# Kernel tuning notes

Hardware: AMD Instinct MI355X
Metric: run time of the kernel (lower is better)

Reference implementation:

```python
import jax, jax.numpy as jnp
import numpy as np

NUM_EMBEDDINGS = 1024
EMBEDDING_DIM = 256
COMMITMENT_COST = 0.25
DECAY = 0.99
EPSILON = 1e-05


def setup_inputs() -> dict:
    key = jax.random.key(0)
    k1, k2, k3 = jax.random.split(key, 3)
    z_e = jax.random.normal(k1, (32, 32, 32, EMBEDDING_DIM), dtype=jnp.float32)
    embedding = jax.random.normal(k2, (NUM_EMBEDDINGS, EMBEDDING_DIM), dtype=jnp.float32)
    ema_cluster_size = jnp.zeros((NUM_EMBEDDINGS,), dtype=jnp.float32)
    ema_w = jax.random.normal(k3, (NUM_EMBEDDINGS, EMBEDDING_DIM), dtype=jnp.float32)
    return {"z_e": z_e, "embedding": embedding,
            "ema_cluster_size": ema_cluster_size, "ema_w": ema_w}


def reference(z_e, embedding, ema_cluster_size, ema_w):
    K, D = embedding.shape
    flat = z_e.reshape(-1, D)  # [N, D]
    distances = (jnp.sum(flat * flat, axis=1, keepdims=True)
                 - 2.0 * (flat @ embedding.T)
                 + jnp.sum(embedding * embedding, axis=1))
    encoding_indices = jnp.argmin(distances, axis=1)  # [N]
    # one_hot @ embedding == gather of nearest codes
    z_q = embedding[encoding_indices].reshape(z_e.shape)

    # EMA codebook update (training branch, torch no_grad)
    counts = jax.ops.segment_sum(jnp.ones_like(encoding_indices, dtype=flat.dtype),
                                 encoding_indices, num_segments=K)  # encodings.sum(0)
    dw = jax.ops.segment_sum(flat, encoding_indices, num_segments=K)  # encodings.T @ flat
    new_cluster_size = DECAY * ema_cluster_size + (1.0 - DECAY) * counts
    new_ema_w = DECAY * ema_w + (1.0 - DECAY) * dw
    n = jnp.sum(new_cluster_size)
    cluster_size = (new_cluster_size + EPSILON) / (n + K * EPSILON) * n
    new_embedding = new_ema_w / cluster_size[:, None]

    codebook_loss = jnp.mean((z_q - jax.lax.stop_gradient(z_e)) ** 2)
    commitment_loss = COMMITMENT_COST * jnp.mean((z_e - jax.lax.stop_gradient(z_q)) ** 2)
    vq_loss = codebook_loss + commitment_loss
    z_q_st = z_e + jax.lax.stop_gradient(z_q - z_e)  # straight-through
    return (z_q_st, vq_loss, encoding_indices,
            new_embedding, new_cluster_size, new_ema_w)
```

## Files before the change

kernel.cpp:

```cpp
#include <hip/hip_runtime.h>

#define DECAY_F 0.99f
#define OMD_F   0.01f
#define EPS_F   1e-5f

typedef __attribute__((ext_vector_type(8)))  __bf16 bf16x8;
typedef __attribute__((ext_vector_type(16))) float  f32x16;

#define WSB_CNTI     0
#define WSB_LOSS     4096
#define WSB_DWACC    8192
#define WSB_CSUM     1056768
#define WSB_ENORM    1056832
#define WSB_IDX      1060928
#define WSB_EHI      1192000
#define WSB_ELO      1716288
#define WSB_SORT     2240576
#define WSB_CURS     2371648

#define OUT_ZQ    0
#define OUT_LOSS  8388608
#define OUT_IDX   8388609
#define OUT_EMB   8421377
#define OUT_CS    8683521
#define OUT_EMAW  8684545

__device__ __forceinline__ unsigned short f2bf(float x) {
    unsigned u = __builtin_bit_cast(unsigned, x);
    u += 0x7fffu + ((u >> 16) & 1u);
    return (unsigned short)(u >> 16);
}
__device__ __forceinline__ float bf2f(unsigned short h) {
    return __builtin_bit_cast(float, (unsigned)h << 16);
}
__device__ __forceinline__ void split8(const float4 a, const float4 b,
                                       uint4& hi, uint4& lo) {
    float f[8] = {a.x, a.y, a.z, a.w, b.x, b.y, b.z, b.w};
    unsigned short h[8], l[8];
    #pragma unroll
    for (int i = 0; i < 8; ++i) {
        h[i] = f2bf(f[i]);
        l[i] = f2bf(f[i] - bf2f(h[i]));
    }
    hi.x = (unsigned)h[0] | ((unsigned)h[1] << 16);
    hi.y = (unsigned)h[2] | ((unsigned)h[3] << 16);
    hi.z = (unsigned)h[4] | ((unsigned)h[5] << 16);
    hi.w = (unsigned)h[6] | ((unsigned)h[7] << 16);
    lo.x = (unsigned)l[0] | ((unsigned)l[1] << 16);
    lo.y = (unsigned)l[2] | ((unsigned)l[3] << 16);
    lo.z = (unsigned)l[4] | ((unsigned)l[5] << 16);
    lo.w = (unsigned)l[6] | ((unsigned)l[7] << 16);
}

__global__ __launch_bounds__(256)
void esplit_enorm_kernel(const float* __restrict__ emb,
                         unsigned short* __restrict__ e_hi,
                         unsigned short* __restrict__ e_lo,
                         float* __restrict__ enorm,
                         float* __restrict__ dwacc,
                         int* __restrict__ cnt,
                         float* __restrict__ lossbuf) {
    const int tid = threadIdx.x, lane = tid & 63, wv = tid >> 6;
    const int gthread = blockIdx.x * 256 + tid;

    *(float4*)(dwacc + (size_t)gthread * 4) = make_float4(0.f, 0.f, 0.f, 0.f);
    if (gthread < 1024) cnt[gthread] = 0;
    if (gthread < 256)  lossbuf[gthread] = 0.f;

    if (gthread < 32768) {
        const int F     = gthread;
        const int chunk = F >> 6;
        const int lh6   = (F >> 5) & 1;
        const int l31f  = F & 31;
        const int g     = chunk >> 4;
        const int kc    = (chunk >> 1) & 7;
        const int kk    = chunk & 1;
        const int k     = g * 32 + l31f;
        const int d0    = kc * 32 + (kk * 2 + lh6) * 8;
        const float4 v0 = *(const float4*)(emb + (size_t)k * 256 + d0);
        const float4 v1 = *(const float4*)(emb + (size_t)k * 256 + d0 + 4);
        uint4 h, l;
        split8(v0, v1, h, l);
        *(uint4*)((char*)e_hi + (size_t)F * 16) = h;
        *(uint4*)((char*)e_lo + (size_t)F * 16) = l;
    }

    const int k = blockIdx.x * 4 + wv;
    const float4 v = *(const float4*)(emb + (size_t)k * 256 + lane * 4);
    float s = v.x * v.x + v.y * v.y + v.z * v.z + v.w * v.w;
    #pragma unroll
    for (int off = 32; off > 0; off >>= 1) s += __shfl_down(s, off);
    if (lane == 0) enorm[k] = s;
}

__global__ __launch_bounds__(256, 2)
void argmin_kernel(const float* __restrict__ z,
                   const unsigned short* __restrict__ e_hi,
                   const unsigned short* __restrict__ e_lo,
                   const float* __restrict__ enorm,
                   const float* __restrict__ emb,
                   int* __restrict__ idx, float* __restrict__ idxf,
                   float* __restrict__ out_zq, int* __restrict__ cnt) {
    __shared__ unsigned short Ah[32 * 512], Al[32 * 512];

    const int tid  = threadIdx.x;
    const int lane = tid & 63;
    const int wv   = tid >> 6;
    const int l31  = lane & 31, lh = lane >> 5;
    const int row0 = blockIdx.x * 64;

    #pragma unroll
    for (int c8 = 0; c8 < 8; ++c8) {
        const int C  = wv * 8 + c8;
        const int i  = C >> 4, kc = (C >> 1) & 7, kk = C & 1;
        const int row = row0 + i * 32 + l31;
        const int d0  = kc * 32 + (kk * 2 + lh) * 8;
        const float4 v0 = *(const float4*)(z + (size_t)row * 256 + d0);
        const float4 v1 = *(const float4*)(z + (size_t)row * 256 + d0 + 4);
        uint4 h, l;
        split8(v0, v1, h, l);
        *(uint4*)((char*)Ah + (size_t)C * 1024 + lane * 16) = h;
        *(uint4*)((char*)Al + (size_t)C * 1024 + lane * 16) = l;
    }
    __syncthreads();

    f32x16 acc[2][2];
    #pragma unroll
    for (int i = 0; i < 2; ++i)
        #pragma unroll
        for (int j = 0; j < 2; ++j) acc[i][j] = (f32x16)0.0f;

    float bestd[2][16];
    int   besti[2][16];
    #pragma unroll
    for (int i = 0; i < 2; ++i)
        #pragma unroll
        for (int r = 0; r < 16; ++r) { bestd[i][r] = 3.4e38f; besti[i][r] = 0; }

    uint4 b0h[4], b0l[4], b1h[4], b1l[4];
    auto loadB = [&](int s, uint4* bh, uint4* bl) {
        const int csp = s >> 3, kc = s & 7;
        #pragma unroll
        for (int j = 0; j < 2; ++j)
            #pragma unroll
            for (int kk = 0; kk < 2; ++kk) {
                const int chunk = (csp * 8 + wv * 2 + j) * 16 + kc * 2 + kk;
                bh[j * 2 + kk] = *(const uint4*)((const char*)e_hi + (size_t)chunk * 1024 + lane * 16);
                bl[j * 2 + kk] = *(const uint4*)((const char*)e_lo + (size_t)chunk * 1024 + lane * 16);
            }
    };
    auto compute = [&](int s, const uint4* bh4, const uint4* bl4) {
        const int kc = s & 7;
        #pragma unroll
        for (int kk = 0; kk < 2; ++kk) {
            bf16x8 bh[2], bl[2];
            #pragma unroll
            for (int j = 0; j < 2; ++j) {
                bh[j] = __builtin_bit_cast(bf16x8, bh4[j * 2 + kk]);
                bl[j] = __builtin_bit_cast(bf16x8, bl4[j * 2 + kk]);
            }
            #pragma unroll
            for (int i = 0; i < 2; ++i) {
                const int C = i * 16 + kc * 2 + kk;
                const bf16x8 ah = __builtin_bit_cast(bf16x8,
                    *(const uint4*)((const char*)Ah + (size_t)C * 1024 + lane * 16));
                const bf16x8 al = __builtin_bit_cast(bf16x8,
                    *(const uint4*)((const char*)Al + (size_t)C * 1024 + lane * 16));
                #pragma unroll
                for (int j = 0; j < 2; ++j) {
                    acc[i][j] = __builtin_amdgcn_mfma_f32_32x32x16_bf16(ah, bh[j], acc[i][j], 0, 0, 0);
                    acc[i][j] = __builtin_amdgcn_mfma_f32_32x32x16_bf16(al, bh[j], acc[i][j], 0, 0, 0);
                    acc[i][j] = __builtin_amdgcn_mfma_f32_32x32x16_bf16(ah, bl[j], acc[i][j], 0, 0, 0);
                }
            }
        }
        if ((s & 7) == 7) {
            const int csp = s >> 3;
            #pragma unroll
            for (int j = 0; j < 2; ++j) {
                const int col = csp * 256 + wv * 64 + j * 32 + l31;
                const float en = enorm[col];
                #pragma unroll
                for (int i = 0; i < 2; ++i)
                    #pragma unroll
                    for (int r = 0; r < 16; ++r) {
                        const float d = fmaf(-2.0f, acc[i][j][r], en);
                        if (d < bestd[i][r] || (d == bestd[i][r] && col < besti[i][r])) {
                            bestd[i][r] = d; besti[i][r] = col;
                        }
                    }
            }
            #pragma unroll
            for (int i = 0; i < 2; ++i)
                #pragma unroll
                for (int j = 0; j < 2; ++j) acc[i][j] = (f32x16)0.0f;
        }
    };

    loadB(0, b0h, b0l);
    for (int s = 0; s < 32; s += 2) {
        loadB(s + 1, b1h, b1l);
        compute(s, b0h, b0l);
        if (s + 2 < 32) loadB(s + 2, b0h, b0l);
        compute(s + 1, b1h, b1l);
    }

    #pragma unroll
    for (int m = 1; m < 32; m <<= 1) {
        #pragma unroll
        for (int i = 0; i < 2; ++i)
            #pragma unroll
            for (int r = 0; r < 16; ++r) {
                const float od = __shfl_xor(bestd[i][r], m);
                const int   oi = __shfl_xor(besti[i][r], m);
                if (od < bestd[i][r] || (od == bestd[i][r] && oi < besti[i][r])) {
                    bestd[i][r] = od; besti[i][r] = oi;
                }
            }
    }

    __syncthreads();
    float* mg_d = (float*)Ah;
    int*   mg_i = (int*)Ah + 256;
    if (l31 == 0) {
        #pragma unroll
        for (int i = 0; i < 2; ++i)
            #pragma unroll
            for (int r = 0; r < 16; ++r) {
                const int rloc = i * 32 + (r & 3) + 8 * (r >> 2) + 4 * lh;
                mg_d[wv * 64 + rloc] = bestd[i][r];
                mg_i[wv * 64 + rloc] = besti[i][r];
            }
    }
    __syncthreads();
    if (tid < 64) {
        float d0 = mg_d[tid];
        int   i0 = mg_i[tid];
        #pragma unroll
        for (int w = 1; w < 4; ++w) {
            const float dw = mg_d[w * 64 + tid];
            const int   iw = mg_i[w * 64 + tid];
            if (dw < d0 || (dw == d0 && iw < i0)) { d0 = dw; i0 = iw; }
        }
        const int n = row0 + tid;
        idx[n] = i0; idxf[n] = (float)i0;
        atomicAdd(&cnt[i0], 1);
        mg_i[tid] = i0;
    }
    __syncthreads();

    #pragma unroll 4
    for (int r = 0; r < 16; ++r) {
        const int row = wv * 16 + r;
        const int code = mg_i[row];
        const float4 e4 = *(const float4*)(emb + (size_t)code * 256 + lane * 4);
        *(float4*)(out_zq + (size_t)(row0 + row) * 256 + lane * 4) = e4;
    }
}

__global__ __launch_bounds__(1024)
void scan_kernel(const float* __restrict__ ema_cs, const int* __restrict__ cnt,
                 float* __restrict__ out_cs, float* __restrict__ csum,
                 int* __restrict__ cursor) {
    __shared__ int   wtmp[16];
    __shared__ float wred[16];
    const int t = threadIdx.x, lane = t & 63, wv = t >> 6;
    const int c = cnt[t];
    const float f = DECAY_F * ema_cs[t] + OMD_F * (float)c;
    out_cs[t] = f;
    float fs = f;
    #pragma unroll
    for (int o = 32; o > 0; o >>= 1) fs += __shfl_down(fs, o);
    if (lane == 0) wred[wv] = fs;
    int v = c;
    #pragma unroll
    for (int o = 1; o < 64; o <<= 1) { const int u = __shfl_up(v, o); if (lane >= o) v += u; }
    if (lane == 63) wtmp[wv] = v;
    __syncthreads();
    if (t == 0) { float s2 = 0.f; for (int w = 0; w < 16; ++w) s2 += wred[w]; csum[0] = s2; }
    int wbase = 0;
    #pragma unroll
    for (int w = 0; w < 16; ++w) if (w < wv) wbase += wtmp[w];
    cursor[t] = wbase + v - c;
}

__global__ __launch_bounds__(256)
void scatter_kernel(const int* __restrict__ idx, int* __restrict__ cursor,
                    int* __restrict__ sorted) {
    const int n = blockIdx.x * 256 + threadIdx.x;
    const int k = idx[n];
    const int p = atomicAdd(&cursor[k], 1);
    sorted[p] = n;
}

__global__ __launch_bounds__(256)
void dw_kernel(const float* __restrict__ z, const float* __restrict__ emb,
               const float* __restrict__ enorm,
               const int* __restrict__ sorted, const int* __restrict__ idx,
               float* __restrict__ dwacc, float* __restrict__ lossbuf) {
    const int lane = threadIdx.x & 63;
    const int w    = blockIdx.x * 4 + (threadIdx.x >> 6);
    const int r0   = w * 16;
    const int srow = sorted[r0 + (lane & 15)];
    const int skey = idx[srow];

    float4 s = make_float4(0.f, 0.f, 0.f, 0.f);
    float sumsq = 0.f;
    int cntr = 0;
    int krun = __shfl(skey, 0);

    auto flush = [&](int k) {
        const float4 e = *(const float4*)(emb + (size_t)k * 256 + lane * 4);
        float val = sumsq - 2.0f * (e.x * s.x + e.y * s.y + e.z * s.z + e.w * s.w);
        #pragma unroll
        for (int off = 32; off > 0; off >>= 1) val += __shfl_down(val, off);
        if (lane == 0) atomicAdd(&lossbuf[k & 255], val + (float)cntr * enorm[k]);
        float* p = dwacc + (size_t)k * 256 + lane * 4;
        atomicAdd(p + 0, s.x); atomicAdd(p + 1, s.y);
        atomicAdd(p + 2, s.z); atomicAdd(p + 3, s.w);
    };

    #pragma unroll 8
    for (int j = 0; j < 16; ++j) {
        const int row = __shfl(srow, j);
        const int k   = __shfl(skey, j);
        if (k != krun) {
            flush(krun);
            s = make_float4(0.f, 0.f, 0.f, 0.f);
            sumsq = 0.f; cntr = 0; krun = k;
        }
        const float4 v = *(const float4*)(z + (size_t)row * 256 + lane * 4);
        s.x += v.x; s.y += v.y; s.z += v.z; s.w += v.w;
        sumsq += v.x * v.x + v.y * v.y + v.z * v.z + v.w * v.w;
        ++cntr;
    }
    flush(krun);
}

__global__ __launch_bounds__(256)
void update_w_kernel(const float* __restrict__ ema_w, const float* __restrict__ dwacc,
                     const float* __restrict__ out_cs, const float* __restrict__ csum,
                     const float* __restrict__ lossbuf,
                     float* __restrict__ out_emb, float* __restrict__ out_emaw,
                     float* __restrict__ out_loss) {
    __shared__ float red[256];
    const int t = threadIdx.x;
    if (blockIdx.x == 0) {
        red[t] = lossbuf[t]; __syncthreads();
        #pragma unroll
        for (int off = 128; off > 0; off >>= 1) {
            if (t < off) red[t] += red[t + off];
            __syncthreads();
        }
        if (t == 0) out_loss[0] = 1.25f * red[0] / 8388608.0f;
    }

    const int g = blockIdx.x * 256 + t;
    const int k = g >> 6;
    const float n_total = csum[0];
    const float cs = (out_cs[k] + EPS_F) / (n_total + 1024.0f * EPS_F) * n_total;

    const float4 w4 = *(const float4*)(ema_w + (size_t)g * 4);
    const float4 d4 = *(const float4*)(dwacc + (size_t)g * 4);
    float4 nw, ne;
    nw.x = DECAY_F * w4.x + OMD_F * d4.x;
    nw.y = DECAY_F * w4.y + OMD_F * d4.y;
    nw.z = DECAY_F * w4.z + OMD_F * d4.z;
    nw.w = DECAY_F * w4.w + OMD_F * d4.w;
    ne.x = nw.x / cs; ne.y = nw.y / cs; ne.z = nw.z / cs; ne.w = nw.w / cs;
    *(float4*)(out_emaw + (size_t)g * 4) = nw;
    *(float4*)(out_emb  + (size_t)g * 4) = ne;
}

extern "C" void kernel_launch(void* const* d_in, const int* in_sizes, int n_in,
                              void* d_out, int out_size, void* d_ws, size_t ws_size,
                              hipStream_t stream) {
    const float* z      = (const float*)d_in[0];
    const float* emb    = (const float*)d_in[1];
    const float* ema_cs = (const float*)d_in[2];
    const float* ema_w  = (const float*)d_in[3];

    float* out = (float*)d_out;
    char*  wsb = (char*)d_ws;

    int*            cnt     = (int*)(wsb + WSB_CNTI);
    float*          lossbuf = (float*)(wsb + WSB_LOSS);
    float*          dwacc   = (float*)(wsb + WSB_DWACC);
    float*          csum    = (float*)(wsb + WSB_CSUM);
    float*          enorm   = (float*)(wsb + WSB_ENORM);
    int*            idx     = (int*)(wsb + WSB_IDX);
    unsigned short* e_hi    = (unsigned short*)(wsb + WSB_EHI);
    unsigned short* e_lo    = (unsigned short*)(wsb + WSB_ELO);
    int*            sorted  = (int*)(wsb + WSB_SORT);
    int*            cursor  = (int*)(wsb + WSB_CURS);

    float* out_zq   = out + OUT_ZQ;
    float* out_loss = out + OUT_LOSS;
    float* out_idxf = out + OUT_IDX;
    float* out_emb  = out + OUT_EMB;
    float* out_cs   = out + OUT_CS;
    float* out_emaw = out + OUT_EMAW;

    esplit_enorm_kernel<<<256, 256, 0, stream>>>(emb, e_hi, e_lo, enorm,
                                                 dwacc, cnt, lossbuf);
    argmin_kernel<<<512, 256, 0, stream>>>(z, e_hi, e_lo, enorm, emb,
                                           idx, out_idxf, out_zq, cnt);
    scan_kernel<<<1, 1024, 0, stream>>>(ema_cs, cnt, out_cs, csum, cursor);
    scatter_kernel<<<128, 256, 0, stream>>>(idx, cursor, sorted);
    dw_kernel<<<512, 256, 0, stream>>>(z, emb, enorm, sorted, idx, dwacc, lossbuf);
    update_w_kernel<<<256, 256, 0, stream>>>(ema_w, dwacc, out_cs, csum, lossbuf,
                                             out_emb, out_emaw, out_loss);
}
```

Baseline: 206.9 us.

## Fuse scan into argmin via last-block ticket and reorder MFMA issue

Removes the separate single-block scan kernel. The last argmin block to finish, found with an atomic ticket, now computes cluster sizes, their sum and the prefix-sum cursors. The MFMA loop is also reordered so all A fragments load first and independent accumulators interleave, with precomputed base pointers and a partial unroll of the stage loop. This saves one launch and its gap and may improve MFMA issue, at the cost of a serialized tail in one block and higher register pressure.

```diff
diff --git a/kernel.cpp b/kernel.cpp
--- a/kernel.cpp
+++ b/kernel.cpp
@@ -11,6 +11,7 @@
 #define WSB_LOSS     4096
 #define WSB_DWACC    8192
 #define WSB_CSUM     1056768
+#define WSB_TICKET   1056772
 #define WSB_ENORM    1056832
 #define WSB_IDX      1060928
 #define WSB_EHI      1192000
@@ -59,13 +60,15 @@
                          float* __restrict__ enorm,
                          float* __restrict__ dwacc,
                          int* __restrict__ cnt,
-                         float* __restrict__ lossbuf) {
+                         float* __restrict__ lossbuf,
+                         int* __restrict__ ticket) {
     const int tid = threadIdx.x, lane = tid & 63, wv = tid >> 6;
     const int gthread = blockIdx.x * 256 + tid;
 
     *(float4*)(dwacc + (size_t)gthread * 4) = make_float4(0.f, 0.f, 0.f, 0.f);
     if (gthread < 1024) cnt[gthread] = 0;
     if (gthread < 256)  lossbuf[gthread] = 0.f;
+    if (gthread == 0)   *ticket = 0;
 
     if (gthread < 32768) {
         const int F     = gthread;
@@ -99,8 +102,11 @@
                    const unsigned short* __restrict__ e_lo,
                    const float* __restrict__ enorm,
                    const float* __restrict__ emb,
+                   const float* __restrict__ ema_cs,
                    int* __restrict__ idx, float* __restrict__ idxf,
-                   float* __restrict__ out_zq, int* __restrict__ cnt) {
+                   float* __restrict__ out_zq, int* __restrict__ cnt,
+                   float* __restrict__ out_cs, float* __restrict__ csum,
+                   int* __restrict__ cursor, int* __restrict__ ticket) {
     __shared__ unsigned short Ah[32 * 512], Al[32 * 512];
 
     const int tid  = threadIdx.x;
@@ -124,6 +130,9 @@
     }
     __syncthreads();
 
+    const char* AhL = (const char*)Ah + lane * 16;
+    const char* AlL = (const char*)Al + lane * 16;
+
     f32x16 acc[2][2];
     #pragma unroll
     for (int i = 0; i < 2; ++i)
@@ -138,22 +147,24 @@
         for (int r = 0; r < 16; ++r) { bestd[i][r] = 3.4e38f; besti[i][r] = 0; }
 
     uint4 b0h[4], b0l[4], b1h[4], b1l[4];
+    const char* ehW = (const char*)e_hi + (size_t)(wv * 2) * 16384 + lane * 16;
+    const char* elW = (const char*)e_lo + (size_t)(wv * 2) * 16384 + lane * 16;
     auto loadB = [&](int s, uint4* bh, uint4* bl) {
         const int csp = s >> 3, kc = s & 7;
         #pragma unroll
         for (int j = 0; j < 2; ++j)
             #pragma unroll
             for (int kk = 0; kk < 2; ++kk) {
-                const int chunk = (csp * 8 + wv * 2 + j) * 16 + kc * 2 + kk;
-                bh[j * 2 + kk] = *(const uint4*)((const char*)e_hi + (size_t)chunk * 1024 + lane * 16);
-                bl[j * 2 + kk] = *(const uint4*)((const char*)e_lo + (size_t)chunk * 1024 + lane * 16);
+                const int off = csp * 131072 + j * 16384 + kc * 2048 + kk * 1024;
+                bh[j * 2 + kk] = *(const uint4*)(ehW + off);
+                bl[j * 2 + kk] = *(const uint4*)(elW + off);
             }
     };
     auto compute = [&](int s, const uint4* bh4, const uint4* bl4) {
         const int kc = s & 7;
         #pragma unroll
         for (int kk = 0; kk < 2; ++kk) {
-            bf16x8 bh[2], bl[2];
+            bf16x8 ah[2], al[2], bh[2], bl[2];
             #pragma unroll
             for (int j = 0; j < 2; ++j) {
                 bh[j] = __builtin_bit_cast(bf16x8, bh4[j * 2 + kk]);
@@ -162,17 +173,24 @@
             #pragma unroll
             for (int i = 0; i < 2; ++i) {
                 const int C = i * 16 + kc * 2 + kk;
-                const bf16x8 ah = __builtin_bit_cast(bf16x8,
-                    *(const uint4*)((const char*)Ah + (size_t)C * 1024 + lane * 16));
-                const bf16x8 al = __builtin_bit_cast(bf16x8,
-                    *(const uint4*)((const char*)Al + (size_t)C * 1024 + lane * 16));
+                ah[i] = __builtin_bit_cast(bf16x8, *(const uint4*)(AhL + C * 1024));
+                al[i] = __builtin_bit_cast(bf16x8, *(const uint4*)(AlL + C * 1024));
+            }
+            #pragma unroll
+            for (int j = 0; j < 2; ++j)
                 #pragma unroll
-                for (int j = 0; j < 2; ++j) {
-                    acc[i][j] = __builtin_amdgcn_mfma_f32_32x32x16_bf16(ah, bh[j], acc[i][j], 0, 0, 0);
-                    acc[i][j] = __builtin_amdgcn_mfma_f32_32x32x16_bf16(al, bh[j], acc[i][j], 0, 0, 0);
-                    acc[i][j] = __builtin_amdgcn_mfma_f32_32x32x16_bf16(ah, bl[j], acc[i][j], 0, 0, 0);
-                }
-            }
+                for (int i = 0; i < 2; ++i)
+                    acc[i][j] = __builtin_amdgcn_mfma_f32_32x32x16_bf16(ah[i], bh[j], acc[i][j], 0, 0, 0);
+            #pragma unroll
+            for (int j = 0; j < 2; ++j)
+                #pragma unroll
+                for (int i = 0; i < 2; ++i)
+                    acc[i][j] = __builtin_amdgcn_mfma_f32_32x32x16_bf16(al[i], bh[j], acc[i][j], 0, 0, 0);
+            #pragma unroll
+            for (int j = 0; j < 2; ++j)
+                #pragma unroll
+                for (int i = 0; i < 2; ++i)
+                    acc[i][j] = __builtin_amdgcn_mfma_f32_32x32x16_bf16(ah[i], bl[j], acc[i][j], 0, 0, 0);
         }
         if ((s & 7) == 7) {
             const int csp = s >> 3;
@@ -198,6 +216,7 @@
     };
 
     loadB(0, b0h, b0l);
+    #pragma unroll 4
     for (int s = 0; s < 32; s += 2) {
         loadB(s + 1, b1h, b1l);
         compute(s, b0h, b0l);
@@ -256,32 +275,44 @@
         const float4 e4 = *(const float4*)(emb + (size_t)code * 256 + lane * 4);
         *(float4*)(out_zq + (size_t)(row0 + row) * 256 + lane * 4) = e4;
     }
-}
-
-__global__ __launch_bounds__(1024)
-void scan_kernel(const float* __restrict__ ema_cs, const int* __restrict__ cnt,
-                 float* __restrict__ out_cs, float* __restrict__ csum,
-                 int* __restrict__ cursor) {
-    __shared__ int   wtmp[16];
-    __shared__ float wred[16];
-    const int t = threadIdx.x, lane = t & 63, wv = t >> 6;
-    const int c = cnt[t];
-    const float f = DECAY_F * ema_cs[t] + OMD_F * (float)c;
-    out_cs[t] = f;
-    float fs = f;
-    #pragma unroll
-    for (int o = 32; o > 0; o >>= 1) fs += __shfl_down(fs, o);
-    if (lane == 0) wred[wv] = fs;
-    int v = c;
-    #pragma unroll
-    for (int o = 1; o < 64; o <<= 1) { const int u = __shfl_up(v, o); if (lane >= o) v += u; }
-    if (lane == 63) wtmp[wv] = v;
+
+    __shared__ int slast;
+    if (tid == 0) {
+        __threadfence();
+        const int t = __hip_atomic_fetch_add(ticket, 1, __ATOMIC_ACQ_REL,
+                                             __HIP_MEMORY_SCOPE_AGENT);
+        slast = (t == 511);
+    }
     __syncthreads();
-    if (t == 0) { float s2 = 0.f; for (int w = 0; w < 16; ++w) s2 += wred[w]; csum[0] = s2; }
-    int wbase = 0;
-    #pragma unroll
-    for (int w = 0; w < 16; ++w) if (w < wv) wbase += wtmp[w];
-    cursor[t] = wbase + v - c;
+    if (slast) {
+        __shared__ int   swi[4];
+        __shared__ float swf[4];
+        int c[4]; int ls = 0; float fsum = 0.f;
+        #pragma unroll
+        for (int i = 0; i < 4; ++i) {
+            c[i] = __hip_atomic_load(&cnt[tid * 4 + i], __ATOMIC_RELAXED,
+                                     __HIP_MEMORY_SCOPE_AGENT);
+            const float f = DECAY_F * ema_cs[tid * 4 + i] + OMD_F * (float)c[i];
+            out_cs[tid * 4 + i] = f;
+            ls += c[i]; fsum += f;
+        }
+        int v = ls;
+        #pragma unroll
+        for (int o = 1; o < 64; o <<= 1) { const int u = __shfl_up(v, o); if (lane >= o) v += u; }
+        float fs = fsum;
+        #pragma unroll
+        for (int o = 32; o > 0; o >>= 1) fs += __shfl_down(fs, o);
+        if (lane == 63) swi[wv] = v;
+        if (lane == 0)  swf[wv] = fs;
+        __syncthreads();
+        if (tid == 0) csum[0] = swf[0] + swf[1] + swf[2] + swf[3];
+        int wbase = 0;
+        #pragma unroll
+        for (int w = 0; w < 4; ++w) if (w < wv) wbase += swi[w];
+        int base = wbase + v - ls;
+        #pragma unroll
+        for (int i = 0; i < 4; ++i) { cursor[tid * 4 + i] = base; base += c[i]; }
+    }
 }
 
 __global__ __launch_bounds__(256)
@@ -387,6 +418,7 @@
     float*          lossbuf = (float*)(wsb + WSB_LOSS);
     float*          dwacc   = (float*)(wsb + WSB_DWACC);
     float*          csum    = (float*)(wsb + WSB_CSUM);
+    int*            ticket  = (int*)(wsb + WSB_TICKET);
     float*          enorm   = (float*)(wsb + WSB_ENORM);
     int*            idx     = (int*)(wsb + WSB_IDX);
     unsigned short* e_hi    = (unsigned short*)(wsb + WSB_EHI);
@@ -402,10 +434,10 @@
     float* out_emaw = out + OUT_EMAW;
 
     esplit_enorm_kernel<<<256, 256, 0, stream>>>(emb, e_hi, e_lo, enorm,
-                                                 dwacc, cnt, lossbuf);
-    argmin_kernel<<<512, 256, 0, stream>>>(z, e_hi, e_lo, enorm, emb,
-                                           idx, out_idxf, out_zq, cnt);
-    scan_kernel<<<1, 1024, 0, stream>>>(ema_cs, cnt, out_cs, csum, cursor);
+                                                 dwacc, cnt, lossbuf, ticket);
+    argmin_kernel<<<512, 256, 0, stream>>>(z, e_hi, e_lo, enorm, emb, ema_cs,
+                                           idx, out_idxf, out_zq, cnt,
+                                           out_cs, csum, cursor, ticket);
     scatter_kernel<<<128, 256, 0, stream>>>(idx, cursor, sorted);
     dw_kernel<<<512, 256, 0, stream>>>(z, emb, enorm, sorted, idx, dwacc, lossbuf);
     update_w_kernel<<<256, 256, 0, stream>>>(ema_w, dwacc, out_cs, csum, lossbuf,
```

New measurement: 302.9 us. 46.4% more time.
